# Optimization experiments

Hardware: AMD Instinct MI355X
Metric: run time of the kernel (lower is better)

Reference implementation:

```python
import jax, jax.numpy as jnp
import numpy as np

B, C, L, T = 8, 512, 2048, 64

def setup_inputs() -> dict:
    key = jax.random.key(0)
    k1, k2, k3 = jax.random.split(key, 3)
    x = jax.random.normal(k1, (B, C, 1, L), dtype=jnp.float32)
    W1 = jax.random.normal(k2, (T, C), dtype=jnp.float32) * (1.0 / np.sqrt(C))
    W2 = jax.random.normal(k3, (T, C), dtype=jnp.float32) * (1.0 / np.sqrt(C))
    gamma = jnp.ones((1, 1), dtype=jnp.float32)
    ranges = 0  # unused by forward
    return {"x": x, "W1": W1, "W2": W2, "gamma": gamma, "ranges": ranges}

def reference(x, W1, W2, gamma, ranges):
    temp = x[:, :, 0, :]                                  # (B, C, L)
    q = jnp.einsum('tc,bcl->btl', W1, temp)               # conv1x1 -> (B, T, L)
    k = jnp.einsum('tc,bcl->btl', W2, temp)               # conv1x1 -> (B, T, L)
    scores = jnp.einsum('btl,btm->blm', q, k)             # Q^T K -> (B, L, L)
    attn = jax.nn.softmax(scores, axis=2)                 # softmax over last dim
    # temp @ attn^T: out[:, :, j] = sum_i attn[j, i] * temp[:, :, i]
    out = jnp.einsum('bci,bji->bcj', temp, attn)          # (B, C, L)
    out = temp + gamma[0, 0] * out                        # gamma scale + residual
    return out[:, :, None, :]                             # (B, C, 1, L)
```

## Files before the change

kernel.cpp:

```cpp
#include <hip/hip_runtime.h>
#include <cstddef>

#define BB 8
#define CC 512
#define LL 2048
#define TT 64

typedef short short8 __attribute__((ext_vector_type(8)));
typedef float floatx4 __attribute__((ext_vector_type(4)));
typedef unsigned short b16u;
typedef unsigned int u32;

static __device__ __forceinline__ unsigned f2bfu(float f) {
    unsigned u = __float_as_uint(f);
    u += 0x7fffu + ((u >> 16) & 1u);
    return u >> 16;
}
static __device__ __forceinline__ float bfu2f(unsigned h) {
    return __uint_as_float(h << 16);
}

#define MFMA16(a, b, c) __builtin_amdgcn_mfma_f32_16x16x32_bf16((a), (b), (c), 0, 0, 0)

static __device__ __forceinline__ void gl2lds16(const void* g, void* l) {
    __builtin_amdgcn_global_load_lds(
        (const __attribute__((address_space(1))) u32*)g,
        (__attribute__((address_space(3))) u32*)l, 16, 0, 0);
}

__global__ __launch_bounds__(256) void wcvt_kernel(
    const float* __restrict__ W1, const float* __restrict__ W2,
    b16u* __restrict__ W1h, b16u* __restrict__ W1l,
    b16u* __restrict__ W2h, b16u* __restrict__ W2l)
{
    int flat = blockIdx.x * 256 + threadIdx.x;
    float4 v1 = *(const float4*)(W1 + (size_t)flat * 4);
    float4 v2 = *(const float4*)(W2 + (size_t)flat * 4);
    const float* e1 = (const float*)&v1;
    const float* e2 = (const float*)&v2;
    unsigned h1[4], l1[4], h2[4], l2[4];
#pragma unroll
    for (int k = 0; k < 4; ++k) {
        h1[k] = f2bfu(e1[k]); l1[k] = f2bfu(e1[k] - bfu2f(h1[k]));
        h2[k] = f2bfu(e2[k]); l2[k] = f2bfu(e2[k] - bfu2f(h2[k]));
    }
    uint2 a, b, c, d;
    a.x = h1[0] | (h1[1] << 16); a.y = h1[2] | (h1[3] << 16);
    b.x = l1[0] | (l1[1] << 16); b.y = l1[2] | (l1[3] << 16);
    c.x = h2[0] | (h2[1] << 16); c.y = h2[2] | (h2[3] << 16);
    d.x = l2[0] | (l2[1] << 16); d.y = l2[2] | (l2[3] << 16);
    *(uint2*)(W1h + (size_t)flat * 4) = a;
    *(uint2*)(W1l + (size_t)flat * 4) = b;
    *(uint2*)(W2h + (size_t)flat * 4) = c;
    *(uint2*)(W2l + (size_t)flat * 4) = d;
}

__global__ __launch_bounds__(256) void qkcvt_kernel(
    const float* __restrict__ x,
    const b16u* __restrict__ W1h, const b16u* __restrict__ W1l,
    const b16u* __restrict__ W2h, const b16u* __restrict__ W2l,
    b16u* __restrict__ Qt, b16u* __restrict__ Kt)
{
    __shared__ b16u Sxh[64 * 72];
    __shared__ b16u Sxl[64 * 72];
    __shared__ b16u S1h[64 * 72];
    __shared__ b16u S1l[64 * 72];
    __shared__ b16u S2h[64 * 72];
    __shared__ b16u S2l[64 * 72];
    const int b  = blockIdx.y;
    const int l0 = blockIdx.x * 64;
    const int tid = threadIdx.x;
    const int lane = tid & 63;
    const int w = tid >> 6;
    const int n16 = lane & 15;
    const int qd = lane >> 4;
    const float* xb = x + (size_t)b * CC * LL;

    const int cx = tid >> 2;
    const int sx = tid & 3;

    float4 xreg[4];
#pragma unroll
    for (int p = 0; p < 4; ++p)
        xreg[p] = *(const float4*)(xb + (size_t)cx * LL + l0 + (sx * 4 + p) * 4);

    floatx4 aq[4], ak[4];
#pragma unroll
    for (int nt = 0; nt < 4; ++nt) {
        aq[nt] = (floatx4){0.f, 0.f, 0.f, 0.f};
        ak[nt] = (floatx4){0.f, 0.f, 0.f, 0.f};
    }

    for (int c0 = 0; c0 < 512; c0 += 64) {
        __syncthreads();
#pragma unroll
        for (int p = 0; p < 4; ++p) {
            const float* e = (const float*)&xreg[p];
            int lbase = (sx * 4 + p) * 4;
#pragma unroll
            for (int k = 0; k < 4; ++k) {
                unsigned h = f2bfu(e[k]);
                unsigned lo = f2bfu(e[k] - bfu2f(h));
                Sxh[(lbase + k) * 72 + cx] = (b16u)h;
                Sxl[(lbase + k) * 72 + cx] = (b16u)lo;
            }
        }
#pragma unroll
        for (int p = 0; p < 2; ++p) {
            int flat = tid + p * 256;
            int t = flat >> 3, s8 = flat & 7;
            size_t off = (size_t)t * 512 + c0 + s8 * 8;
            *(uint4*)&S1h[t * 72 + s8 * 8] = *(const uint4*)(W1h + off);
            *(uint4*)&S1l[t * 72 + s8 * 8] = *(const uint4*)(W1l + off);
            *(uint4*)&S2h[t * 72 + s8 * 8] = *(const uint4*)(W2h + off);
            *(uint4*)&S2l[t * 72 + s8 * 8] = *(const uint4*)(W2l + off);
        }
        __syncthreads();
        if (c0 < 448) {
#pragma unroll
            for (int p = 0; p < 4; ++p)
                xreg[p] = *(const float4*)(xb + (size_t)(c0 + 64 + cx) * LL +
                                           l0 + (sx * 4 + p) * 4);
        }
#pragma unroll
        for (int kc = 0; kc < 2; ++kc) {
            const int ao = (w * 16 + n16) * 72 + kc * 32 + qd * 8;
            short8 a1h = *(const short8*)&S1h[ao];
            short8 a1l = *(const short8*)&S1l[ao];
            short8 a2h = *(const short8*)&S2h[ao];
            short8 a2l = *(const short8*)&S2l[ao];
#pragma unroll
            for (int nt = 0; nt < 4; ++nt) {
                const int bo = (nt * 16 + n16) * 72 + kc * 32 + qd * 8;
                short8 bh = *(const short8*)&Sxh[bo];
                short8 bl = *(const short8*)&Sxl[bo];
                aq[nt] = MFMA16(a1h, bh, aq[nt]);
                aq[nt] = MFMA16(a1h, bl, aq[nt]);
                aq[nt] = MFMA16(a1l, bh, aq[nt]);
                ak[nt] = MFMA16(a2h, bh, ak[nt]);
                ak[nt] = MFMA16(a2h, bl, ak[nt]);
                ak[nt] = MFMA16(a2l, bh, ak[nt]);
            }
        }
    }
#pragma unroll
    for (int nt = 0; nt < 4; ++nt) {
        int l = l0 + nt * 16 + n16;
        uint2 pq, pk;
        pq.x = f2bfu(aq[nt][0]) | (f2bfu(aq[nt][1]) << 16);
        pq.y = f2bfu(aq[nt][2]) | (f2bfu(aq[nt][3]) << 16);
        pk.x = f2bfu(ak[nt][0]) | (f2bfu(ak[nt][1]) << 16);
        pk.y = f2bfu(ak[nt][2]) | (f2bfu(ak[nt][3]) << 16);
        *(uint2*)(Qt + ((size_t)(b * 2048) + l) * 64 + w * 16 + qd * 4) = pq;
        *(uint2*)(Kt + ((size_t)(b * 2048) + l) * 64 + w * 16 + qd * 4) = pk;
    }
}

__global__ __launch_bounds__(256) void xcvt_kernel(
    const float* __restrict__ x, b16u* __restrict__ XT)
{
    const int b = blockIdx.z, c0 = blockIdx.y * 64, it = blockIdx.x;
    const int tid = threadIdx.x;
#pragma unroll
    for (int p = 0; p < 4; ++p) {
        int flat = tid + p * 256;
        int c = flat >> 4, s = flat & 15;
        float4 v = *(const float4*)(x + ((size_t)(b * 512) + c0 + c) * 2048 + it * 64 + s * 4);
        uint2 wv;
        wv.x = f2bfu(v.x) | (f2bfu(v.y) << 16);
        wv.y = f2bfu(v.z) | (f2bfu(v.w) << 16);
        int phys = (((s >> 1) ^ (c & 7)) << 3) + ((s & 1) << 2);
        *(uint2*)(XT + (((size_t)(b * 32) + it) * 512 + c0 + c) * 64 + phys) = wv;
    }
}

__global__ __launch_bounds__(256) void pexp_kernel(
    const b16u* __restrict__ Qt, const b16u* __restrict__ Kt,
    b16u* __restrict__ P, float* __restrict__ Zpart, int b_off)
{
    __shared__ b16u Ks[64 * 72];
    __shared__ b16u Ls[64 * 68];
    __shared__ float Zw[4][64];
    const int pb = blockIdx.z, b = b_off + pb;
    const int j0 = blockIdx.y * 64;
    const int ibase = blockIdx.x * 1024;
    const int tid = threadIdx.x;
    const int lane = tid & 63;
    const int w = tid >> 6;
    const int n16 = lane & 15;
    const int qd = lane >> 4;
    const b16u* kb = Kt + (size_t)b * (2048 * 64);

    short8 qf[4][2];
#pragma unroll
    for (int nt = 0; nt < 4; ++nt)
#pragma unroll
        for (int kc = 0; kc < 2; ++kc)
            qf[nt][kc] = *(const short8*)(Qt +
                ((size_t)(b * 2048) + j0 + nt * 16 + n16) * 64 + kc * 32 + qd * 8);

    uint4 kreg[2];
#pragma unroll
    for (int p = 0; p < 2; ++p) {
        int flat = tid + p * 256;
        kreg[p] = *(const uint4*)(kb + (size_t)(ibase + (flat >> 3)) * 64 + (flat & 7) * 8);
    }
    float zacc[4] = {0.f, 0.f, 0.f, 0.f};

    for (int it = 0; it < 16; ++it) {
#pragma unroll
        for (int p = 0; p < 2; ++p) {
            int flat = tid + p * 256;
            *(uint4*)&Ks[(flat >> 3) * 72 + (flat & 7) * 8] = kreg[p];
        }
        {
            const int itn = (it + 1 < 16) ? it + 1 : 15;
#pragma unroll
            for (int p = 0; p < 2; ++p) {
                int flat = tid + p * 256;
                kreg[p] = *(const uint4*)(kb +
                    (size_t)(ibase + itn * 64 + (flat >> 3)) * 64 + (flat & 7) * 8);
            }
        }
        __syncthreads();
        floatx4 sacc[4];
#pragma unroll
        for (int nt = 0; nt < 4; ++nt) sacc[nt] = (floatx4){0.f, 0.f, 0.f, 0.f};
#pragma unroll
        for (int kc = 0; kc < 2; ++kc) {
            short8 af = *(const short8*)&Ks[(w * 16 + n16) * 72 + kc * 32 + qd * 8];
#pragma unroll
            for (int nt = 0; nt < 4; ++nt)
                sacc[nt] = MFMA16(af, qf[nt][kc], sacc[nt]);
        }
#pragma unroll
        for (int nt = 0; nt < 4; ++nt) {
            float p0 = __expf(sacc[nt][0] - 20.0f);
            float p1 = __expf(sacc[nt][1] - 20.0f);
            float p2 = __expf(sacc[nt][2] - 20.0f);
            float p3 = __expf(sacc[nt][3] - 20.0f);
            zacc[nt] += (p0 + p1) + (p2 + p3);
            uint2 pk;
            pk.x = f2bfu(p0) | (f2bfu(p1) << 16);
            pk.y = f2bfu(p2) | (f2bfu(p3) << 16);
            *(uint2*)&Ls[(nt * 16 + n16) * 68 + w * 16 + qd * 4] = pk;
        }
        __syncthreads();
        size_t prow = ((size_t)(pb * 32) + (ibase >> 6) + it) * 2048 + j0;
#pragma unroll
        for (int p = 0; p < 4; ++p) {
            int u = tid + p * 256;
            int row = u >> 4, s = u & 15;
            int phys = (((s >> 1) ^ (row & 7)) << 3) + ((s & 1) << 2);
            *(uint2*)(P + (prow + row) * 64 + phys) = *(const uint2*)&Ls[row * 68 + s * 4];
        }
    }
#pragma unroll
    for (int nt = 0; nt < 4; ++nt) {
        float z = zacc[nt];
        z += __shfl_xor(z, 16);
        z += __shfl_xor(z, 32);
        if (qd == 0) Zw[w][nt * 16 + n16] = z;
    }
    __syncthreads();
    if (tid < 64) {
        float s = Zw[0][tid] + Zw[1][tid] + Zw[2][tid] + Zw[3][tid];
        Zpart[((size_t)blockIdx.x * 8 + b) * 2048 + j0 + tid] = s;
    }
}

__global__ __launch_bounds__(256, 2) void gemm_kernel(
    const float* __restrict__ x, const b16u* __restrict__ XT,
    const b16u* __restrict__ P, const float* __restrict__ Zpart,
    const float* __restrict__ gamma, float* __restrict__ out, int b_off)
{
    __shared__ __align__(16) char smem[69632];
    b16u* As = (b16u*)smem;
    b16u* Bs = (b16u*)(smem + 32768);
    const int pb = blockIdx.z, b = b_off + pb;
    const int j0 = blockIdx.x * 128;
    const int c0 = blockIdx.y * 128;
    const int tid = threadIdx.x;
    const int lane = tid & 63;
    const int w = tid >> 6;
    const int n16 = lane & 15;
    const int qd = lane >> 4;
    const int wc = w & 1;
    const int wj = w >> 1;

    const b16u* tA = XT + ((size_t)(b * 32) * 512 + c0) * 64 + w * 2048 + lane * 8;
    const b16u* tB = P + ((size_t)(pb * 32) * 2048 + j0) * 64 + w * 2048 + lane * 8;
    b16u* lA = As + w * 2048;
    b16u* lB = Bs + w * 2048;

#define STAGE(IT, BUF)                                                    \
    {                                                                      \
        const b16u* ga = tA + (size_t)(IT) * 32768;                        \
        const b16u* gb = tB + (size_t)(IT) * 131072;                       \
        _Pragma("unroll")                                                  \
        for (int ch = 0; ch < 4; ++ch) {                                   \
            gl2lds16(ga + ch * 512, lA + (BUF) * 8192 + ch * 512);         \
            gl2lds16(gb + ch * 512, lB + (BUF) * 8192 + ch * 512);         \
        }                                                                  \
    }

    STAGE(0, 0)
    __syncthreads();

    floatx4 acc[4][4];
#pragma unroll
    for (int mt = 0; mt < 4; ++mt)
#pragma unroll
        for (int nt = 0; nt < 4; ++nt) acc[mt][nt] = (floatx4){0.f, 0.f, 0.f, 0.f};

    for (int it = 0; it < 32; ++it) {
        const int buf = it & 1;
        if (it < 31) STAGE(it + 1, buf ^ 1)
        const b16u* Ab = As + buf * 8192;
        const b16u* Bb = Bs + buf * 8192;
#pragma unroll
        for (int kc = 0; kc < 2; ++kc) {
            const int co = (((kc * 4 + qd) ^ (n16 & 7)) << 3);
            short8 af[4], bf[4];
#pragma unroll
            for (int mt = 0; mt < 4; ++mt)
                af[mt] = *(const short8*)&Ab[(wc * 64 + mt * 16 + n16) * 64 + co];
#pragma unroll
            for (int nt = 0; nt < 4; ++nt)
                bf[nt] = *(const short8*)&Bb[(wj * 64 + nt * 16 + n16) * 64 + co];
#pragma unroll
            for (int mt = 0; mt < 4; ++mt)
#pragma unroll
                for (int nt = 0; nt < 4; ++nt)
                    acc[mt][nt] = MFMA16(af[mt], bf[nt], acc[mt][nt]);
        }
        __syncthreads();
    }
#undef STAGE

    const float g = gamma[0];
    float* st = (float*)(smem + w * 17408);
#pragma unroll
    for (int nt = 0; nt < 4; ++nt) {
        int j = j0 + wj * 64 + nt * 16 + n16;
        float zi = g / (Zpart[(size_t)b * 2048 + j] +
                        Zpart[16384 + (size_t)b * 2048 + j]);
#pragma unroll
        for (int mt = 0; mt < 4; ++mt)
#pragma unroll
            for (int r = 0; r < 4; ++r)
                st[(mt * 16 + qd * 4 + r) * 68 + nt * 16 + n16] = acc[mt][nt][r] * zi;
    }
    __syncthreads();
#pragma unroll
    for (int p = 0; p < 16; ++p) {
        int rl = qd * 16 + p;
        int cg = c0 + wc * 64 + rl;
        size_t go = ((size_t)(b * 512) + cg) * 2048 + j0 + wj * 64 + n16 * 4;
        float4 v = *(const float4*)&st[rl * 68 + n16 * 4];
        float4 xv = *(const float4*)(x + go);
        v.x += xv.x; v.y += xv.y; v.z += xv.z; v.w += xv.w;
        *(float4*)(out + go) = v;
    }
}

extern "C" void kernel_launch(void* const* d_in, const int* in_sizes, int n_in,
                              void* d_out, int out_size, void* d_ws, size_t ws_size,
                              hipStream_t stream)
{
    const float* x     = (const float*)d_in[0];
    const float* W1    = (const float*)d_in[1];
    const float* W2    = (const float*)d_in[2];
    const float* gamma = (const float*)d_in[3];
    float* out = (float*)d_out;

    b16u* Qt  = (b16u*)d_ws;
    b16u* Kt  = Qt  + (size_t)BB * LL * TT;
    b16u* W1h = Kt  + (size_t)BB * LL * TT;
    b16u* W1l = W1h + (size_t)TT * CC;
    b16u* W2h = W1l + (size_t)TT * CC;
    b16u* W2l = W2h + (size_t)TT * CC;
    float* Zp = (float*)(W2l + (size_t)TT * CC);
    b16u* XT  = (b16u*)(Zp + 2 * 8 * 2048);
    b16u* P   = XT + (size_t)BB * 32 * 512 * 64;

    const size_t base = (size_t)((char*)P - (char*)d_ws);
    const size_t pbat = (size_t)LL * LL * 2;
    int nb = 8;
    if (ws_size < base + 8 * pbat) nb = 4;
    if (ws_size < base + 4 * pbat) nb = 2;
    if (ws_size < base + 2 * pbat) nb = 1;

    wcvt_kernel <<<dim3(32),        256, 0, stream>>>(W1, W2, W1h, W1l, W2h, W2l);
    qkcvt_kernel<<<dim3(32, BB),    256, 0, stream>>>(x, W1h, W1l, W2h, W2l, Qt, Kt);
    xcvt_kernel <<<dim3(32, 8, BB), 256, 0, stream>>>(x, XT);
    for (int b0 = 0; b0 < BB; b0 += nb) {
        pexp_kernel<<<dim3(2, 32, nb), 256, 0, stream>>>(Qt, Kt, P, Zp, b0);
        gemm_kernel<<<dim3(16, 4, nb), 256, 0, stream>>>(x, XT, P, Zp, gamma, out, b0);
    }
}
```

Before: 172.1 us.

## Fuse x bf16 transpose into QK kernel, split pexp wider, retile output GEMM

```diff
diff --git a/kernel.cpp b/kernel.cpp
--- a/kernel.cpp
+++ b/kernel.cpp
@@ -59,7 +59,7 @@
     const float* __restrict__ x,
     const b16u* __restrict__ W1h, const b16u* __restrict__ W1l,
     const b16u* __restrict__ W2h, const b16u* __restrict__ W2l,
-    b16u* __restrict__ Qt, b16u* __restrict__ Kt)
+    b16u* __restrict__ Qt, b16u* __restrict__ Kt, b16u* __restrict__ XT)
 {
     __shared__ b16u Sxh[64 * 72];
     __shared__ b16u Sxl[64 * 72];
@@ -68,7 +68,8 @@
     __shared__ b16u S2h[64 * 72];
     __shared__ b16u S2l[64 * 72];
     const int b  = blockIdx.y;
-    const int l0 = blockIdx.x * 64;
+    const int lt = blockIdx.x;
+    const int l0 = lt * 64;
     const int tid = threadIdx.x;
     const int lane = tid & 63;
     const int w = tid >> 6;
@@ -96,14 +97,21 @@
 #pragma unroll
         for (int p = 0; p < 4; ++p) {
             const float* e = (const float*)&xreg[p];
-            int lbase = (sx * 4 + p) * 4;
+            int s = sx * 4 + p;
+            int lbase = s * 4;
+            unsigned h[4];
 #pragma unroll
             for (int k = 0; k < 4; ++k) {
-                unsigned h = f2bfu(e[k]);
-                unsigned lo = f2bfu(e[k] - bfu2f(h));
-                Sxh[(lbase + k) * 72 + cx] = (b16u)h;
+                h[k] = f2bfu(e[k]);
+                unsigned lo = f2bfu(e[k] - bfu2f(h[k]));
+                Sxh[(lbase + k) * 72 + cx] = (b16u)h[k];
                 Sxl[(lbase + k) * 72 + cx] = (b16u)lo;
             }
+            uint2 wv;
+            wv.x = h[0] | (h[1] << 16);
+            wv.y = h[2] | (h[3] << 16);
+            int phys = (((s >> 1) ^ (cx & 7)) << 3) + ((s & 1) << 2);
+            *(uint2*)(XT + (((size_t)(b * 32) + lt) * 512 + c0 + cx) * 64 + phys) = wv;
         }
 #pragma unroll
         for (int p = 0; p < 2; ++p) {
@@ -156,24 +164,6 @@
     }
 }
 
-__global__ __launch_bounds__(256) void xcvt_kernel(
-    const float* __restrict__ x, b16u* __restrict__ XT)
-{
-    const int b = blockIdx.z, c0 = blockIdx.y * 64, it = blockIdx.x;
-    const int tid = threadIdx.x;
-#pragma unroll
-    for (int p = 0; p < 4; ++p) {
-        int flat = tid + p * 256;
-        int c = flat >> 4, s = flat & 15;
-        float4 v = *(const float4*)(x + ((size_t)(b * 512) + c0 + c) * 2048 + it * 64 + s * 4);
-        uint2 wv;
-        wv.x = f2bfu(v.x) | (f2bfu(v.y) << 16);
-        wv.y = f2bfu(v.z) | (f2bfu(v.w) << 16);
-        int phys = (((s >> 1) ^ (c & 7)) << 3) + ((s & 1) << 2);
-        *(uint2*)(XT + (((size_t)(b * 32) + it) * 512 + c0 + c) * 64 + phys) = wv;
-    }
-}
-
 __global__ __launch_bounds__(256) void pexp_kernel(
     const b16u* __restrict__ Qt, const b16u* __restrict__ Kt,
     b16u* __restrict__ P, float* __restrict__ Zpart, int b_off)
@@ -183,7 +173,7 @@
     __shared__ float Zw[4][64];
     const int pb = blockIdx.z, b = b_off + pb;
     const int j0 = blockIdx.y * 64;
-    const int ibase = blockIdx.x * 1024;
+    const int ibase = blockIdx.x * 512;
     const int tid = threadIdx.x;
     const int lane = tid & 63;
     const int w = tid >> 6;
@@ -207,14 +197,14 @@
     }
     float zacc[4] = {0.f, 0.f, 0.f, 0.f};
 
-    for (int it = 0; it < 16; ++it) {
+    for (int it = 0; it < 8; ++it) {
 #pragma unroll
         for (int p = 0; p < 2; ++p) {
             int flat = tid + p * 256;
             *(uint4*)&Ks[(flat >> 3) * 72 + (flat & 7) * 8] = kreg[p];
         }
         {
-            const int itn = (it + 1 < 16) ? it + 1 : 15;
+            const int itn = (it + 1 < 8) ? it + 1 : 7;
 #pragma unroll
             for (int p = 0; p < 2; ++p) {
                 int flat = tid + p * 256;
@@ -269,28 +259,26 @@
     }
 }
 
-__global__ __launch_bounds__(256, 2) void gemm_kernel(
+__global__ __launch_bounds__(128) void gemm_kernel(
     const float* __restrict__ x, const b16u* __restrict__ XT,
     const b16u* __restrict__ P, const float* __restrict__ Zpart,
     const float* __restrict__ gamma, float* __restrict__ out, int b_off)
 {
-    __shared__ __align__(16) char smem[69632];
+    __shared__ __align__(16) char smem[49152];
     b16u* As = (b16u*)smem;
     b16u* Bs = (b16u*)(smem + 32768);
     const int pb = blockIdx.z, b = b_off + pb;
-    const int j0 = blockIdx.x * 128;
+    const int j0 = blockIdx.x * 64;
     const int c0 = blockIdx.y * 128;
     const int tid = threadIdx.x;
     const int lane = tid & 63;
     const int w = tid >> 6;
     const int n16 = lane & 15;
     const int qd = lane >> 4;
-    const int wc = w & 1;
-    const int wj = w >> 1;
-
-    const b16u* tA = XT + ((size_t)(b * 32) * 512 + c0) * 64 + w * 2048 + lane * 8;
+
+    const b16u* tA = XT + ((size_t)(b * 32) * 512 + c0) * 64 + w * 4096 + lane * 8;
     const b16u* tB = P + ((size_t)(pb * 32) * 2048 + j0) * 64 + w * 2048 + lane * 8;
-    b16u* lA = As + w * 2048;
+    b16u* lA = As + w * 4096;
     b16u* lB = Bs + w * 2048;
 
 #define STAGE(IT, BUF)                                                    \
@@ -298,10 +286,11 @@
         const b16u* ga = tA + (size_t)(IT) * 32768;                        \
         const b16u* gb = tB + (size_t)(IT) * 131072;                       \
         _Pragma("unroll")                                                  \
-        for (int ch = 0; ch < 4; ++ch) {                                   \
+        for (int ch = 0; ch < 8; ++ch)                                     \
             gl2lds16(ga + ch * 512, lA + (BUF) * 8192 + ch * 512);         \
-            gl2lds16(gb + ch * 512, lB + (BUF) * 8192 + ch * 512);         \
-        }                                                                  \
+        _Pragma("unroll")                                                  \
+        for (int ch = 0; ch < 4; ++ch)                                     \
+            gl2lds16(gb + ch * 512, lB + (BUF) * 4096 + ch * 512);         \
     }
 
     STAGE(0, 0)
@@ -317,17 +306,17 @@
         const int buf = it & 1;
         if (it < 31) STAGE(it + 1, buf ^ 1)
         const b16u* Ab = As + buf * 8192;
-        const b16u* Bb = Bs + buf * 8192;
+        const b16u* Bb = Bs + buf * 4096;
 #pragma unroll
         for (int kc = 0; kc < 2; ++kc) {
             const int co = (((kc * 4 + qd) ^ (n16 & 7)) << 3);
             short8 af[4], bf[4];
 #pragma unroll
             for (int mt = 0; mt < 4; ++mt)
-                af[mt] = *(const short8*)&Ab[(wc * 64 + mt * 16 + n16) * 64 + co];
+                af[mt] = *(const short8*)&Ab[(w * 64 + mt * 16 + n16) * 64 + co];
 #pragma unroll
             for (int nt = 0; nt < 4; ++nt)
-                bf[nt] = *(const short8*)&Bb[(wj * 64 + nt * 16 + n16) * 64 + co];
+                bf[nt] = *(const short8*)&Bb[(nt * 16 + n16) * 64 + co];
 #pragma unroll
             for (int mt = 0; mt < 4; ++mt)
 #pragma unroll
@@ -342,9 +331,12 @@
     float* st = (float*)(smem + w * 17408);
 #pragma unroll
     for (int nt = 0; nt < 4; ++nt) {
-        int j = j0 + wj * 64 + nt * 16 + n16;
-        float zi = g / (Zpart[(size_t)b * 2048 + j] +
-                        Zpart[16384 + (size_t)b * 2048 + j]);
+        int j = j0 + nt * 16 + n16;
+        float zsum = Zpart[(size_t)b * 2048 + j]
+                   + Zpart[(size_t)(1 * 8 + b) * 2048 + j]
+                   + Zpart[(size_t)(2 * 8 + b) * 2048 + j]
+                   + Zpart[(size_t)(3 * 8 + b) * 2048 + j];
+        float zi = g / zsum;
 #pragma unroll
         for (int mt = 0; mt < 4; ++mt)
 #pragma unroll
@@ -354,9 +346,9 @@
     __syncthreads();
 #pragma unroll
     for (int p = 0; p < 16; ++p) {
-        int rl = qd * 16 + p;
-        int cg = c0 + wc * 64 + rl;
-        size_t go = ((size_t)(b * 512) + cg) * 2048 + j0 + wj * 64 + n16 * 4;
+        int rl = p * 4 + qd;
+        int cg = c0 + w * 64 + rl;
+        size_t go = ((size_t)(b * 512) + cg) * 2048 + j0 + n16 * 4;
         float4 v = *(const float4*)&st[rl * 68 + n16 * 4];
         float4 xv = *(const float4*)(x + go);
         v.x += xv.x; v.y += xv.y; v.z += xv.z; v.w += xv.w;
@@ -381,7 +373,7 @@
     b16u* W2h = W1l + (size_t)TT * CC;
     b16u* W2l = W2h + (size_t)TT * CC;
     float* Zp = (float*)(W2l + (size_t)TT * CC);
-    b16u* XT  = (b16u*)(Zp + 2 * 8 * 2048);
+    b16u* XT  = (b16u*)(Zp + 4 * 8 * 2048);
     b16u* P   = XT + (size_t)BB * 32 * 512 * 64;
 
     const size_t base = (size_t)((char*)P - (char*)d_ws);
@@ -391,11 +383,10 @@
     if (ws_size < base + 4 * pbat) nb = 2;
     if (ws_size < base + 2 * pbat) nb = 1;
 
-    wcvt_kernel <<<dim3(32),        256, 0, stream>>>(W1, W2, W1h, W1l, W2h, W2l);
-    qkcvt_kernel<<<dim3(32, BB),    256, 0, stream>>>(x, W1h, W1l, W2h, W2l, Qt, Kt);
-    xcvt_kernel <<<dim3(32, 8, BB), 256, 0, stream>>>(x, XT);
+    wcvt_kernel <<<dim3(32),     256, 0, stream>>>(W1, W2, W1h, W1l, W2h, W2l);
+    qkcvt_kernel<<<dim3(32, BB), 256, 0, stream>>>(x, W1h, W1l, W2h, W2l, Qt, Kt, XT);
     for (int b0 = 0; b0 < BB; b0 += nb) {
-        pexp_kernel<<<dim3(2, 32, nb), 256, 0, stream>>>(Qt, Kt, P, Zp, b0);
-        gemm_kernel<<<dim3(16, 4, nb), 256, 0, stream>>>(x, XT, P, Zp, gamma, out, b0);
-    }
-}
+        pexp_kernel<<<dim3(4, 32, nb), 256, 0, stream>>>(Qt, Kt, P, Zp, b0);
+        gemm_kernel<<<dim3(32, 4, nb), 128, 0, stream>>>(x, XT, P, Zp, gamma, out, b0);
+    }
+}
```

Measured after the change: 198.3 us. 1.15x slower.
